# Performance work log

Measured on AMD Instinct MI355X. Metric: run time of the kernel, lower is better.

## Reference

```python
import jax, jax.numpy as jnp
import numpy as np

B, S, E, H, C = 2, 2048, 1024, 16, 16
SQ2 = np.float32(np.sqrt(2.0))


def setup_inputs() -> dict:
    key = jax.random.key(0)
    ks = jax.random.split(key, 32)
    sc = 0.02
    d = {"query": jax.random.normal(ks[0], (B, S, E), jnp.float32)}
    i = 1
    for dom in ("f", "w", "c"):
        d[f"Wp_{dom}"] = jax.random.normal(ks[i], (E, E), jnp.float32) * sc; i += 1
        d[f"bp_{dom}"] = jnp.zeros((E,), jnp.float32)
        d[f"Wc_{dom}"] = jax.random.normal(ks[i], (C, E, 3), jnp.float32) * sc; i += 1
        d[f"bc_{dom}"] = jnp.zeros((C,), jnp.float32)
        d["F" + dom] = jax.random.normal(ks[i], (C, E), jnp.float32); i += 1
    d["mha_iw"] = jax.random.normal(ks[i], (3 * E, E), jnp.float32) * sc; i += 1
    d["mha_ib"] = jnp.zeros((3 * E,), jnp.float32)
    d["mha_ow"] = jax.random.normal(ks[i], (E, E), jnp.float32) * sc; i += 1
    d["mha_ob"] = jnp.zeros((E,), jnp.float32)
    d["fus_W"] = jax.random.normal(ks[i], (E, 3 * E), jnp.float32) * sc; i += 1
    d["fus_b"] = jnp.zeros((E,), jnp.float32)
    return d


def _conv1d(x, W, b):
    # x: [B,S,E] real -> [B,S,C], conv over sequence, kernel 3, same padding
    y = jax.lax.conv_general_dilated(x.transpose(0, 2, 1), W, (1,), [(1, 1)],
                                     dimension_numbers=("NCH", "OIH", "NCH"))
    return (y + b[None, :, None]).transpose(0, 2, 1)


def _channels(x, Wc, bc, Fp):
    # spectral conv (real/imag separately if complex) + adaptive softmax filtering
    if jnp.iscomplexobj(x):
        ch = _conv1d(x.real, Wc, bc) + 1j * _conv1d(x.imag, Wc, bc)
    else:
        ch = _conv1d(x, Wc, bc)
    fw = jax.nn.softmax(Fp, axis=0)  # [C,E], softmax over channels
    return jnp.einsum("bsc,ce->bse", ch, fw.astype(ch.dtype))


def _spec_attn(q, k, v):
    scale = np.float32(1.0) / jnp.sqrt(jnp.asarray(q.shape[-1], jnp.float32))
    scores = jnp.einsum("bse,bte->bst", q, k) * scale
    if jnp.iscomplexobj(scores):
        w = jax.nn.softmax(scores.real, axis=-1)
        cw = (w * jnp.exp(1j * jnp.angle(scores))).astype(jnp.complex64)
        return jnp.einsum("bst,bte->bse", cw, v)
    return jnp.einsum("bst,bte->bse", jax.nn.softmax(scores, axis=-1), v)


def _haar(x):
    # simplified Haar wavelet transform; S is a power of 2 so no padding needed
    cur, coeffs = x, []
    while cur.shape[1] > 1:
        e, o = cur[:, 0::2, :], cur[:, 1::2, :]
        coeffs.append((e - o) / SQ2)
        cur = (e + o) / SQ2
    coeffs.append(cur)
    return jnp.concatenate(coeffs[::-1], axis=1)


def _dct_mats(L):
    n = jnp.arange(L, dtype=jnp.float32)
    k = n[:, None]
    D = jnp.cos(np.pi * k * (2.0 * n + 1.0) / (2.0 * L))
    D = D.at[0].multiply(np.float32(np.sqrt(1.0 / L)))
    D = D.at[1:].multiply(np.float32(np.sqrt(2.0 / L)))
    I = jnp.cos(np.pi * n * (2.0 * k + 1.0) / (2.0 * L))
    I = I.at[:, 0].multiply(np.float32(np.sqrt(1.0 / L)))
    I = I.at[:, 1:].multiply(np.float32(np.sqrt(2.0 / L)))
    return D, I


def _domain(x, Wp, bp, Wc, bc, Fp, domain):
    # key=value=query so q_domain == k_domain == v_domain
    xd = x @ Wp.T + bp
    if domain == "fourier":
        s = jnp.fft.fft(xd, axis=1)
        ch = _channels(s, Wc, bc, Fp)
        out = _spec_attn(ch, ch, ch)
        return jnp.fft.ifft(out, axis=1).real
    elif domain == "wavelet":
        s = _haar(xd)
        ch = _channels(s, Wc, bc, Fp)
        return _spec_attn(ch, ch, ch)  # inverse wavelet is identity in source
    else:  # cosine
        D, I = _dct_mats(xd.shape[1])
        s = jnp.einsum("st,bte->bse", D, xd)
        ch = _channels(s, Wc, bc, Fp)
        out = _spec_attn(ch, ch, ch)
        return jnp.einsum("st,bte->bse", I, out)


def _mha(x, iw, ib, ow, ob, nheads):
    # torch nn.MultiheadAttention (batch_first) self-attention
    Bx, L, Ex = x.shape
    hd = Ex // nheads
    qkv = x @ iw.T + ib
    q, k, v = jnp.split(qkv, 3, axis=-1)
    sh = lambda t: t.reshape(Bx, L, nheads, hd).transpose(0, 2, 1, 3)
    q, k, v = sh(q), sh(k), sh(v)
    a = jax.nn.softmax(jnp.einsum("bhld,bhmd->bhlm", q, k) / np.float32(np.sqrt(hd)), axis=-1)
    o = jnp.einsum("bhlm,bhmd->bhld", a, v).transpose(0, 2, 1, 3).reshape(Bx, L, Ex)
    return o @ ow.T + ob


def reference(query, Wp_f, bp_f, Wc_f, bc_f, Ff, Wp_w, bp_w, Wc_w, bc_w, Fw,
              Wp_c, bp_c, Wc_c, bc_c, Fc, mha_iw, mha_ib, mha_ow, mha_ob, fus_W, fus_b):
    outs = [
        _domain(query, Wp_f, bp_f, Wc_f, bc_f, Ff, "fourier"),
        _domain(query, Wp_w, bp_w, Wc_w, bc_w, Fw, "wavelet"),
        _domain(query, Wp_c, bp_c, Wc_c, bc_c, Fc, "cosine"),
    ]
    Bq, Sq, Eq = query.shape
    stacked = jnp.stack(outs, axis=2)                 # [B,S,3,E]
    corr = _mha(stacked.reshape(Bq * Sq, 3, Eq), mha_iw, mha_ib, mha_ow, mha_ob, H)
    fused = corr.reshape(Bq, Sq, 3 * Eq)              # concat of correlated domain outputs
    return fused @ fus_W.T + fus_b
```

## Files before the change

kernel.cpp:

```cpp
#include <hip/hip_runtime.h>
#include <cmath>

#define BB 2
#define SS_ 2048
#define EE 1024
#define CC 16

typedef __attribute__((ext_vector_type(8))) short short8v;
typedef __attribute__((ext_vector_type(4))) float floatx4;

__device__ __forceinline__ void split4(const float4 v, short4& h, short4& l)
{
    unsigned ux = __float_as_uint(v.x), uy = __float_as_uint(v.y);
    unsigned uz = __float_as_uint(v.z), uw = __float_as_uint(v.w);
    h.x = (short)(ux >> 16); h.y = (short)(uy >> 16);
    h.z = (short)(uz >> 16); h.w = (short)(uw >> 16);
    float lx = v.x - __uint_as_float(ux & 0xFFFF0000u);
    float ly = v.y - __uint_as_float(uy & 0xFFFF0000u);
    float lz = v.z - __uint_as_float(uz & 0xFFFF0000u);
    float lw = v.w - __uint_as_float(uw & 0xFFFF0000u);
    l.x = (short)(__float_as_uint(lx) >> 16);
    l.y = (short)(__float_as_uint(ly) >> 16);
    l.z = (short)(__float_as_uint(lz) >> 16);
    l.w = (short)(__float_as_uint(lw) >> 16);
}

#define BM 128
#define BN 128
#define BK 32
#define LDP 40

__launch_bounds__(256, 2)
__global__ void gemm_at(const float* __restrict__ A, const float* __restrict__ Bsrc,
                        float* __restrict__ C,
                        int K, int lda, int ldb, int ldc,
                        long sA, long sB, long sC, float alpha, int KS)
{
    __shared__ short sAh[BM * LDP], sAl[BM * LDP], sBh[BN * LDP], sBl[BN * LDP];
    const int z = blockIdx.z;
    const int bz = z / KS, ks = z % KS;
    const int klen = K / KS, kbase = ks * klen;
    A += (size_t)bz * sA; Bsrc += (size_t)bz * sB; C += (size_t)bz * sC;
    const int tid = threadIdx.x;
    const int m0 = blockIdx.y * BM, n0 = blockIdx.x * BN;

    const int lr0 = tid >> 3;
    const int kc0 = (tid & 7) * 4;
// ... 69 lines not shown
    }

    #pragma unroll
    for (int i = 0; i < 4; ++i) {
        const int mbase = m0 + wm * 64 + i * 16 + qd * 4;
        #pragma unroll
        for (int j = 0; j < 4; ++j) {
            const int n = n0 + wn * 64 + j * 16 + lr;
            #pragma unroll
            for (int r = 0; r < 4; ++r)
                atomicAdd(&C[(size_t)(mbase + r) * ldc + n], alpha * acc[i][j][r]);
        }
    }
}

template<int NT, int MODE>
__launch_bounds__(256, 4)
__global__ void skmfma(const float* __restrict__ A0, const float* __restrict__ A1,
                       const float* __restrict__ B0, const float* __restrict__ B1,
                       float* __restrict__ C0, float* __restrict__ C1,
                       int K, int lda, int ldb, int ldc,
                       long sA, long sB, long sC, float alpha, int KS)
{
    constexpr int NA = (MODE >= 1) ? 2 : 1;
    constexpr int NB = (MODE == 2) ? 2 : 1;
    constexpr int NACC = (MODE == 1) ? 2 : 1;
    constexpr int CT = NT / 16;
    __shared__ short sAh[NA][64 * 40], sAl[NA][64 * 40];
    __shared__ short sBh[NB][NT * 40], sBl[NB][NT * 40];
    const int z = blockIdx.z;
    const int zb = z / KS, ks = z % KS;
    const int klen = K / KS, kbase = ks * klen;
    const float* Ap[NA]; const float* Bp[NB]; float* Cp[NACC];
    Ap[0] = A0 + (size_t)zb * sA;
    if constexpr (NA == 2) Ap[1] = A1 + (size_t)zb * sA;
    Bp[0] = B0 + (size_t)zb * sB;
    if constexpr (NB == 2) Bp[1] = B1 + (size_t)zb * sB;
    Cp[0] = C0 + (size_t)zb * sC;
    if constexpr (NACC == 2) Cp[1] = C1 + (size_t)zb * sC;

    const int tid = threadIdx.x;
    const int m0 = blockIdx.x * 64;
    const int arow = tid >> 2, akc = (tid & 3) * 8;
    const int lane = tid & 63, w = tid >> 6;
    const int lr = lane & 15, qd = lane >> 4;

    floatx4 acc[NACC][CT];
    #pragma unroll
    for (int s = 0; s < NACC; ++s)
        #pragma unroll
        for (int j = 0; j < CT; ++j)
            acc[s][j] = (floatx4){0.f, 0.f, 0.f, 0.f};

    for (int kc = 0; kc < klen; kc += 32) {
        __syncthreads();
        #pragma unroll
        for (int s = 0; s < NA; ++s) {
            const float* pa = Ap[s] + (size_t)(m0 + arow) * lda + kbase + kc + akc;
            float4 v0 = *(const float4*)pa;
            float4 v1 = *(const float4*)(pa + 4);
            short4 h, l;
            split4(v0, h, l);
            *(short4*)&sAh[s][arow * 40 + akc] = h;
            *(short4*)&sAl[s][arow * 40 + akc] = l;
            split4(v1, h, l);
            *(short4*)&sAh[s][arow * 40 + akc + 4] = h;
            *(short4*)&sAl[s][arow * 40 + akc + 4] = l;
        }
        #pragma unroll
        for (int s = 0; s < NB; ++s) {
            for (int lin = tid; lin < 32 * (NT / 4); lin += 256) {
                int kk = lin / (NT / 4), n4 = (lin % (NT / 4)) * 4;
                float4 v = *(const float4*)(Bp[s] + (size_t)(kbase + kc + kk) * ldb + n4);
                short4 h, l; split4(v, h, l);
                sBh[s][(n4 + 0) * 40 + kk] = h.x; sBh[s][(n4 + 1) * 40 + kk] = h.y;
                sBh[s][(n4 + 2) * 40 + kk] = h.z; sBh[s][(n4 + 3) * 40 + kk] = h.w;
                sBl[s][(n4 + 0) * 40 + kk] = l.x; sBl[s][(n4 + 1) * 40 + kk] = l.y;
                sBl[s][(n4 + 2) * 40 + kk] = l.z; sBl[s][(n4 + 3) * 40 + kk] = l.w;
            }
        }
        __syncthreads();
        short8v ah[NA], alv[NA];
        #pragma unroll
        for (int s = 0; s < NA; ++s) {
            ah[s]  = *(const short8v*)&sAh[s][(w * 16 + lr) * 40 + qd * 8];
            alv[s] = *(const short8v*)&sAl[s][(w * 16 + lr) * 40 + qd * 8];
        }
        short8v bh[NB][CT], bl[NB][CT];
        #pragma unroll
        for (int s = 0; s < NB; ++s)
            #pragma unroll
            for (int j = 0; j < CT; ++j) {
                bh[s][j] = *(const short8v*)&sBh[s][(j * 16 + lr) * 40 + qd * 8];
                bl[s][j] = *(const short8v*)&sBl[s][(j * 16 + lr) * 40 + qd * 8];
            }
        if constexpr (MODE == 0) {
            #pragma unroll
            for (int j = 0; j < CT; ++j) {
                acc[0][j] = __builtin_amdgcn_mfma_f32_16x16x32_bf16(ah[0], bh[0][j], acc[0][j], 0, 0, 0);
                acc[0][j] = __builtin_amdgcn_mfma_f32_16x16x32_bf16(ah[0], bl[0][j], acc[0][j], 0, 0, 0);
                acc[0][j] = __builtin_amdgcn_mfma_f32_16x16x32_bf16(alv[0], bh[0][j], acc[0][j], 0, 0, 0);
            }
        } else if constexpr (MODE == 1) {
            #pragma unroll
            for (int j = 0; j < CT; ++j) {
                acc[0][j] = __builtin_amdgcn_mfma_f32_16x16x32_bf16(ah[0], bh[0][j], acc[0][j], 0, 0, 0);
                acc[0][j] = __builtin_amdgcn_mfma_f32_16x16x32_bf16(ah[0], bl[0][j], acc[0][j], 0, 0, 0);
                acc[0][j] = __builtin_amdgcn_mfma_f32_16x16x32_bf16(alv[0], bh[0][j], acc[0][j], 0, 0, 0);
                acc[1][j] = __builtin_amdgcn_mfma_f32_16x16x32_bf16(ah[1], bh[0][j], acc[1][j], 0, 0, 0);
                acc[1][j] = __builtin_amdgcn_mfma_f32_16x16x32_bf16(ah[1], bl[0][j], acc[1][j], 0, 0, 0);
                acc[1][j] = __builtin_amdgcn_mfma_f32_16x16x32_bf16(alv[1], bh[0][j], acc[1][j], 0, 0, 0);
            }
        } else {
            #pragma unroll
            for (int j = 0; j < CT; ++j) {
                acc[0][j] = __builtin_amdgcn_mfma_f32_16x16x32_bf16(ah[0], bh[0][j], acc[0][j], 0, 0, 0);
                acc[0][j] = __builtin_amdgcn_mfma_f32_16x16x32_bf16(ah[0], bl[0][j], acc[0][j], 0, 0, 0);
                acc[0][j] = __builtin_amdgcn_mfma_f32_16x16x32_bf16(alv[0], bh[0][j], acc[0][j], 0, 0, 0);
                acc[0][j] = __builtin_amdgcn_mfma_f32_16x16x32_bf16(ah[1], bh[1][j], acc[0][j], 0, 0, 0);
                acc[0][j] = __builtin_amdgcn_mfma_f32_16x16x32_bf16(ah[1], bl[1][j], acc[0][j], 0, 0, 0);
                acc[0][j] = __builtin_amdgcn_mfma_f32_16x16x32_bf16(alv[1], bh[1][j], acc[0][j], 0, 0, 0);
            }
        }
    }
    #pragma unroll
    for (int s = 0; s < NACC; ++s)
        #pragma unroll
        for (int j = 0; j < CT; ++j) {
            const int n = j * 16 + lr;
            const int mb = m0 + w * 16 + qd * 4;
            #pragma unroll
            for (int r = 0; r < 4; ++r)
                atomicAdd(&Cp[s][(size_t)(mb + r) * ldc + n], alpha * acc[s][j][r]);
        }
}

__global__ void gen_trig(float* __restrict__ Cc, float* __restrict__ Sn,
                         float* __restrict__ D, float* __restrict__ I)
{
    size_t idx = (size_t)blockIdx.x * 256 + threadIdx.x;
    if (idx < 4194304) {
        int k = (int)(idx >> 11);
        int n = (int)(idx & 2047);
        int m = (k * n) & 2047;
        float ang = (float)(6.283185307179586 * (double)m / 2048.0);
        Cc[idx] = cosf(ang);
        Sn[idx] = -sinf(ang);
    } else {
        idx -= 4194304;
        int i = (int)(idx >> 11);
        int j = (int)(idx & 2047);
        const float r1 = 0.022097086912079608f;
        const float r2 = 0.03125f;
        const float pif = 3.14159265358979323846f;
        float a  = (pif * (float)i) * (float)(2 * j + 1) / 4096.0f;
        D[idx] = cosf(a) * (i == 0 ? r1 : r2);
        float ai = (pif * (float)j) * (float)(2 * i + 1) / 4096.0f;
        I[idx] = cosf(ai) * (j == 0 ? r1 : r2);
    }
}
// ... 257 lines not shown
    #pragma unroll
    for (int c = 0; c < 16; ++c) {
        float cv = scr[row * 17 + c];
        float cvi = cplx ? sci[row * 17 + c] : 0.f;
        #pragma unroll
        for (int j = 0; j < 4; ++j) {
            float g = sG[c * 16 + ln * 4 + j];
            qp[j] = fmaf(cv, g, qp[j]);
            if (cplx) qpi[j] = fmaf(cvi, g, qpi[j]);
        }
    }
    *(float4*)(QR + ro) = *(float4*)&qp[0];
    if (cplx) *(float4*)(QI + ro) = *(float4*)&qpi[0];
}

__launch_bounds__(256)
__global__ void flash_all(const float* __restrict__ QpFr, const float* __restrict__ QpFi,
                          const float* __restrict__ chFr, const float* __restrict__ chFi,
                          float* __restrict__ OFr, float* __restrict__ OFi,
                          const float* __restrict__ QpW, const float* __restrict__ chW,
                          float* __restrict__ Ow_,
                          const float* __restrict__ QpC, const float* __restrict__ chC,
                          float* __restrict__ Oc_)
{
    const int dom = blockIdx.z;
    const int b = blockIdx.y;
    const int w = threadIdx.x >> 6, lane = threadIdx.x & 63;
    const int s = blockIdx.x * 4 + w;
    if (dom != 0) {
        const float* Qp = dom == 1 ? QpW : QpC;
        const float* ch = dom == 1 ? chW : chC;
        float* O = dom == 1 ? Ow_ : Oc_;
        const float* qrow = Qp + ((size_t)(b * 2048 + s)) * 16;
        float q[16];
        #pragma unroll
        for (int j = 0; j < 4; ++j) *(float4*)&q[j * 4] = *(const float4*)(qrow + j * 4);
        const float* chb = ch + (size_t)b * 2048 * 16;
        float m = -3.4e38f, l = 0.f;
        float acc[16] = {};
        for (int t = lane; t < 2048; t += 64) {
            const float* kp = chb + (size_t)t * 16;
            float kv[16];
            #pragma unroll
            for (int j = 0; j < 4; ++j) *(float4*)&kv[j * 4] = *(const float4*)(kp + j * 4);
            float sc = 0.f;
            #pragma unroll
            for (int e = 0; e < 16; ++e) sc = fmaf(q[e], kv[e], sc);
            float mn = fmaxf(m, sc);
            float al = __expf(m - mn), p = __expf(sc - mn);
            l = l * al + p;
            #pragma unroll
            for (int e = 0; e < 16; ++e) acc[e] = fmaf(acc[e], al, p * kv[e]);
            m = mn;
        }
        #pragma unroll
        for (int off = 1; off < 64; off <<= 1) {
            float m2 = __shfl_xor(m, off, 64);
            float l2 = __shfl_xor(l, off, 64);
            float mn = fmaxf(m, m2);
            float ra = __expf(m - mn), rb = __expf(m2 - mn);
            l = l * ra + l2 * rb;
            #pragma unroll
            for (int e = 0; e < 16; ++e) {
                float a2 = __shfl_xor(acc[e], off, 64);
                acc[e] = acc[e] * ra + a2 * rb;
            }
            m = mn;
        }
        if (lane < 4) {
            float inv = 1.f / l;
            float4 o4 = {acc[lane * 4] * inv, acc[lane * 4 + 1] * inv,
                         acc[lane * 4 + 2] * inv, acc[lane * 4 + 3] * inv};
            *(float4*)(O + ((size_t)(b * 2048 + s)) * 16 + lane * 4) = o4;
        }
        return;
    }
    float qr[16], qi[16];
    {
        const float* qrow = QpFr + ((size_t)(b * 2048 + s)) * 16;
        const float* qrowI = QpFi + ((size_t)(b * 2048 + s)) * 16;
        #pragma unroll
        for (int j = 0; j < 4; ++j) {
            *(float4*)&qr[j * 4] = *(const float4*)(qrow + j * 4);
            *(float4*)&qi[j * 4] = *(const float4*)(qrowI + j * 4);
        }
    }
    const float* cbR = chFr + (size_t)b * 2048 * 16;
    const float* cbI = chFi + (size_t)b * 2048 * 16;
    float m = -3.4e38f, l = 0.f;
    float aR[16] = {}, aI[16] = {};
    for (int t = lane; t < 2048; t += 64) {
        float kr[16], ki[16];
        #pragma unroll
        for (int j = 0; j < 4; ++j) {
            *(float4*)&kr[j * 4] = *(const float4*)(cbR + (size_t)t * 16 + j * 4);
            *(float4*)&ki[j * 4] = *(const float4*)(cbI + (size_t)t * 16 + j * 4);
        }
        float sre = 0.f, sim = 0.f;
        #pragma unroll
        for (int e = 0; e < 16; ++e) {
            sre = fmaf(qr[e], kr[e], sre); sre = fmaf(-qi[e], ki[e], sre);
            sim = fmaf(qr[e], ki[e], sim); sim = fmaf(qi[e], kr[e], sim);
        }
        float mn = fmaxf(m, sre);
        float al = __expf(m - mn), p = __expf(sre - mn);
        l = l * al + p;
        float rr = sqrtf(sre * sre + sim * sim);
        float iv = (rr > 0.f) ? (p / rr) : 0.f;
        float wr = (rr > 0.f) ? iv * sre : p;
        float wi = (rr > 0.f) ? iv * sim : 0.f;
        #pragma unroll
        for (int e = 0; e < 16; ++e) {
            aR[e] = fmaf(aR[e], al, wr * kr[e] - wi * ki[e]);
            aI[e] = fmaf(aI[e], al, wr * ki[e] + wi * kr[e]);
        }
        m = mn;
    }
    #pragma unroll
    for (int off = 1; off < 64; off <<= 1) {
        float m2 = __shfl_xor(m, off, 64);
        float l2 = __shfl_xor(l, off, 64);
        float mn = fmaxf(m, m2);
        float ra = __expf(m - mn), rb = __expf(m2 - mn);
        l = l * ra + l2 * rb;
        #pragma unroll
        for (int e = 0; e < 16; ++e) {
            float a2 = __shfl_xor(aR[e], off, 64);
            aR[e] = aR[e] * ra + a2 * rb;
            float b2 = __shfl_xor(aI[e], off, 64);
            aI[e] = aI[e] * ra + b2 * rb;
        }
        m = mn;
    }
    float inv = 1.f / l;
    size_t ro = ((size_t)(b * 2048 + s)) * 16;
    if (lane < 4) {
        float4 o4 = {aR[lane * 4] * inv, aR[lane * 4 + 1] * inv,
                     aR[lane * 4 + 2] * inv, aR[lane * 4 + 3] * inv};
        *(float4*)(OFr + ro + lane * 4) = o4;
    } else if (lane < 8) {
        int j = lane - 4;
        float4 o4 = {aI[j * 4] * inv, aI[j * 4 + 1] * inv,
                     aI[j * 4 + 2] * inv, aI[j * 4 + 3] * inv};
        *(float4*)(OFi + ro + j * 4) = o4;
    }
// ... 140 lines not shown
    float* Rf   = alloc(65536);
    float* Rc   = alloc(65536);
    float* Tw   = alloc(196608);
    float* chFr = alloc(65536); float* chFi = alloc(65536);
    float* QpFr = alloc(65536); float* QpFi = alloc(65536);
    float* chW  = alloc(65536); float* QpW  = alloc(65536);
    float* chC  = alloc(65536); float* QpC  = alloc(65536);
    float* OFr  = alloc(65536); float* OFi  = alloc(65536);
    float* Ow   = alloc(65536); float* Oc   = alloc(65536);
    float* Pt   = alloc(156672);
    float* Mten = alloc(41616);
    float* ybv  = alloc(1024);
    if (ws_size < off * sizeof(float)) return;

    float* Uf = Ucat, *Uw = Ucat + 196608, *Uc = Ucat + 2 * 196608;
    const long SE48 = 2048 * 48, SE16 = 2048 * 16;

    build_w2<<<dim3(576), dim3(256), 0, stream>>>(Wc[0], Wc[1], Wc[2], W2cat);
    prep_fw_G<<<dim3(3), dim3(256), 0, stream>>>(Fp[0], Fp[1], Fp[2], fwT, Gm);
    build_ub2<<<dim3(3), dim3(256), 0, stream>>>(bp[0], bp[1], bp[2], W2cat, ubv);
    build_yb2<<<dim3(256), dim3(256), 0, stream>>>(mha_ob, fus_W, fus_b, ybv);
    gen_trig<<<dim3(32768), dim3(256), 0, stream>>>(MAT0, MAT1, DCTD, DCTI);
    transpose_wp3<<<dim3(32, 32, 3), dim3(256), 0, stream>>>(Wp[0], Wp[1], Wp[2], WpT);
    init_all<<<dim3(34980), dim3(256), 0, stream>>>(W3cat, ubv, Pt, FTb, out, ybv);

    skmfma<48, 0><<<dim3(16, 1, 6), dim3(256), 0, stream>>>(
        WpT, nullptr, W2cat, nullptr, W3cat, nullptr,
        1024, 1024, 48, 48, 1048576, 49152, 49152, 1.f, 2);
    skmfma<48, 0><<<dim3(64, 1, 6), dim3(256), 0, stream>>>(
        query, nullptr, W3cat, nullptr, Ucat, nullptr,
        1024, 1024, 48, 48, 0, 49152, 196608, 1.f, 2);
    skmfma<48, 1><<<dim3(32, 1, 8), dim3(256), 0, stream>>>(
        MAT0, MAT1, Uf, nullptr, Tfr, Tfi,
        2048, 2048, 48, 48, 0, SE48, SE48, 1.f, 4);
    skmfma<48, 0><<<dim3(32, 1, 8), dim3(256), 0, stream>>>(
        DCTD, nullptr, Uc, nullptr, Tc, nullptr,
        2048, 2048, 48, 48, 0, SE48, SE48, 1.f, 4);

    haar_all<<<dim3(12, 2), dim3(256), 0, stream>>>(Uw, Tw);

    conv_all<<<dim3(32, 2, 3), dim3(256), 0, stream>>>(
        Tfr, Tfi, Tw, Tc, Gm, bc[0], bc[1], bc[2],
        chFr, chFi, chW, chC, QpFr, QpFi, QpW, QpC);

    flash_all<<<dim3(512, 2, 3), dim3(256), 0, stream>>>(
        QpFr, QpFi, chFr, chFi, OFr, OFi, QpW, chW, Ow, QpC, chC, Oc);

    skmfma<16, 2><<<dim3(32, 1, 8), dim3(256), 0, stream>>>(
        MAT0, MAT1, OFr, OFi, Rf, nullptr,
        2048, 2048, 16, 16, 0, SE16, SE16, 1.f / 2048.f, 4);
    skmfma<16, 0><<<dim3(32, 1, 8), dim3(256), 0, stream>>>(
        DCTI, nullptr, Oc, nullptr, Rc, nullptr,
        2048, 2048, 16, 16, 0, SE16, SE16, 1.f, 4);
    skmfma<16, 0><<<dim3(48, 1, 6), dim3(256), 0, stream>>>(
        mha_iw, nullptr, fwT, nullptr, Pt, nullptr,
        1024, 1024, 16, 17, 0, 16384, 52224, 1.f, 2);

    ib_append<<<dim3(36), dim3(256), 0, stream>>>(mha_ib, Pt);
    build_M<<<dim3(144), dim3(256), 0, stream>>>(Pt, Mten);

    mha_o<<<dim3(16, 16), dim3(256), 0, stream>>>(Rf, Ow, Rc, Pt, Mten, MO);

    transpose_k<<<dim3(32, 32), dim3(256), 0, stream>>>(mha_ow, OWT, 1024, 1024);
    gemm_at<<<dim3(8, 8, 6), dim3(256), 0, stream>>>(
        fus_W, OWT, FTb, 1024, 3072, 1024, 3072, 1024, 0, 1024, 1.f, 2);

    gemm_at<<<dim3(8, 32, 2), dim3(256), 0, stream>>>(
        MO, FTb, out, 3072, 3072, 3072, 1024, 0, 0, 0, 1.f, 2);
}
```

Before: 765.7 us.

## Merge skinny GEMM launches, restructure flash attention, raise split-K and occupancy

Replaces the templated skinny MFMA kernel with specialized kernels that merge the forward Fourier and DCT transforms, and the inverse transforms plus the MHA projection, into single launches. This cuts launch count and lets the groups run concurrently. The flash attention kernels are rewritten to handle two query rows per wave and to process keys in blocks of 256 with one max rescale per block instead of one per key. The large GEMMs double their split-K factor and raise launch bounds to 4 blocks per SM, which adds atomic traffic and register pressure.

New measurement: 979.3 us. +27.9%, slower.

```diff
diff --git a/kernel.cpp b/kernel.cpp
--- a/kernel.cpp
+++ b/kernel.cpp
@@ -30,7 +30,7 @@
 #define BK 32
 #define LDP 40
 
-__launch_bounds__(256, 2)
+__launch_bounds__(256, 4)
 __global__ void gemm_at(const float* __restrict__ A, const float* __restrict__ Bsrc,
                         float* __restrict__ C,
                         int K, int lda, int ldb, int ldc,
@@ -130,125 +130,281 @@
     }
 }
 
-template<int NT, int MODE>
 __launch_bounds__(256, 4)
-__global__ void skmfma(const float* __restrict__ A0, const float* __restrict__ A1,
-                       const float* __restrict__ B0, const float* __restrict__ B1,
-                       float* __restrict__ C0, float* __restrict__ C1,
-                       int K, int lda, int ldb, int ldc,
-                       long sA, long sB, long sC, float alpha, int KS)
-{
-    constexpr int NA = (MODE >= 1) ? 2 : 1;
-    constexpr int NB = (MODE == 2) ? 2 : 1;
-    constexpr int NACC = (MODE == 1) ? 2 : 1;
-    constexpr int CT = NT / 16;
-    __shared__ short sAh[NA][64 * 40], sAl[NA][64 * 40];
-    __shared__ short sBh[NB][NT * 40], sBl[NB][NT * 40];
+__global__ void sk48(const float* __restrict__ A, const float* __restrict__ B,
+                     float* __restrict__ C, int lda,
+                     long sA, long sB, long sC, int KS)
+{
+    __shared__ short sAh[64 * 40], sAl[64 * 40];
+    __shared__ short sBh[48 * 40], sBl[48 * 40];
     const int z = blockIdx.z;
     const int zb = z / KS, ks = z % KS;
-    const int klen = K / KS, kbase = ks * klen;
-    const float* Ap[NA]; const float* Bp[NB]; float* Cp[NACC];
-    Ap[0] = A0 + (size_t)zb * sA;
-    if constexpr (NA == 2) Ap[1] = A1 + (size_t)zb * sA;
-    Bp[0] = B0 + (size_t)zb * sB;
-    if constexpr (NB == 2) Bp[1] = B1 + (size_t)zb * sB;
-    Cp[0] = C0 + (size_t)zb * sC;
-    if constexpr (NACC == 2) Cp[1] = C1 + (size_t)zb * sC;
-
+    const int kbase = ks * 512;
+    A += (size_t)zb * sA; B += (size_t)zb * sB; C += (size_t)zb * sC;
     const int tid = threadIdx.x;
     const int m0 = blockIdx.x * 64;
     const int arow = tid >> 2, akc = (tid & 3) * 8;
     const int lane = tid & 63, w = tid >> 6;
     const int lr = lane & 15, qd = lane >> 4;
 
-    floatx4 acc[NACC][CT];
-    #pragma unroll
-    for (int s = 0; s < NACC; ++s)
-        #pragma unroll
-        for (int j = 0; j < CT; ++j)
-            acc[s][j] = (floatx4){0.f, 0.f, 0.f, 0.f};
-
-    for (int kc = 0; kc < klen; kc += 32) {
+    floatx4 acc[3];
+    #pragma unroll
+    for (int j = 0; j < 3; ++j) acc[j] = (floatx4){0.f, 0.f, 0.f, 0.f};
+
+    for (int kc = 0; kc < 512; kc += 32) {
         __syncthreads();
-        #pragma unroll
-        for (int s = 0; s < NA; ++s) {
-            const float* pa = Ap[s] + (size_t)(m0 + arow) * lda + kbase + kc + akc;
-            float4 v0 = *(const float4*)pa;
-            float4 v1 = *(const float4*)(pa + 4);
+        {
+            const float* pa = A + (size_t)(m0 + arow) * lda + kbase + kc + akc;
+            float4 v0 = *(const float4*)pa, v1 = *(const float4*)(pa + 4);
             short4 h, l;
             split4(v0, h, l);
-            *(short4*)&sAh[s][arow * 40 + akc] = h;
-            *(short4*)&sAl[s][arow * 40 + akc] = l;
+            *(short4*)&sAh[arow * 40 + akc] = h;
+            *(short4*)&sAl[arow * 40 + akc] = l;
             split4(v1, h, l);
-            *(short4*)&sAh[s][arow * 40 + akc + 4] = h;
-            *(short4*)&sAl[s][arow * 40 + akc + 4] = l;
-        }
-        #pragma unroll
-        for (int s = 0; s < NB; ++s) {
-            for (int lin = tid; lin < 32 * (NT / 4); lin += 256) {
-                int kk = lin / (NT / 4), n4 = (lin % (NT / 4)) * 4;
-                float4 v = *(const float4*)(Bp[s] + (size_t)(kbase + kc + kk) * ldb + n4);
-                short4 h, l; split4(v, h, l);
-                sBh[s][(n4 + 0) * 40 + kk] = h.x; sBh[s][(n4 + 1) * 40 + kk] = h.y;
-                sBh[s][(n4 + 2) * 40 + kk] = h.z; sBh[s][(n4 + 3) * 40 + kk] = h.w;
-                sBl[s][(n4 + 0) * 40 + kk] = l.x; sBl[s][(n4 + 1) * 40 + kk] = l.y;
-                sBl[s][(n4 + 2) * 40 + kk] = l.z; sBl[s][(n4 + 3) * 40 + kk] = l.w;
+            *(short4*)&sAh[arow * 40 + akc + 4] = h;
+            *(short4*)&sAl[arow * 40 + akc + 4] = l;
+        }
+        for (int lin = tid; lin < 384; lin += 256) {
+            int kk = lin / 12, n4 = (lin % 12) * 4;
+            float4 v = *(const float4*)(B + (size_t)(kbase + kc + kk) * 48 + n4);
+            short4 h, l; split4(v, h, l);
+            sBh[(n4 + 0) * 40 + kk] = h.x; sBh[(n4 + 1) * 40 + kk] = h.y;
+            sBh[(n4 + 2) * 40 + kk] = h.z; sBh[(n4 + 3) * 40 + kk] = h.w;
+            sBl[(n4 + 0) * 40 + kk] = l.x; sBl[(n4 + 1) * 40 + kk] = l.y;
+            sBl[(n4 + 2) * 40 + kk] = l.z; sBl[(n4 + 3) * 40 + kk] = l.w;
+        }
+        __syncthreads();
+        short8v ah = *(const short8v*)&sAh[(w * 16 + lr) * 40 + qd * 8];
+        short8v al = *(const short8v*)&sAl[(w * 16 + lr) * 40 + qd * 8];
+        #pragma unroll
+        for (int j = 0; j < 3; ++j) {
+            short8v bh = *(const short8v*)&sBh[(j * 16 + lr) * 40 + qd * 8];
+            short8v bl = *(const short8v*)&sBl[(j * 16 + lr) * 40 + qd * 8];
+            acc[j] = __builtin_amdgcn_mfma_f32_16x16x32_bf16(ah, bh, acc[j], 0, 0, 0);
+            acc[j] = __builtin_amdgcn_mfma_f32_16x16x32_bf16(ah, bl, acc[j], 0, 0, 0);
+            acc[j] = __builtin_amdgcn_mfma_f32_16x16x32_bf16(al, bh, acc[j], 0, 0, 0);
+        }
+    }
+    #pragma unroll
+    for (int j = 0; j < 3; ++j) {
+        const int n = j * 16 + lr;
+        const int mb = m0 + w * 16 + qd * 4;
+        #pragma unroll
+        for (int r = 0; r < 4; ++r)
+            atomicAdd(&C[(size_t)(mb + r) * 48 + n], acc[j][r]);
+    }
+}
+
+__launch_bounds__(256, 4)
+__global__ void skinny_fwd(const float* __restrict__ MAT0, const float* __restrict__ MAT1,
+                           const float* __restrict__ DCTD,
+                           const float* __restrict__ Uf, const float* __restrict__ Uc,
+                           float* __restrict__ Tfr, float* __restrict__ Tfi,
+                           float* __restrict__ Tc)
+{
+    __shared__ short sAh[2][64 * 40], sAl[2][64 * 40];
+    __shared__ short sBh[48 * 40], sBl[48 * 40];
+    const int z = blockIdx.z;
+    const bool dual = (z < 8);
+    const int zz = dual ? z : z - 8;
+    const int zb = zz >> 2, ks = zz & 3;
+    const int kbase = ks * 512;
+    const float* A0 = dual ? MAT0 : DCTD;
+    const float* Bp = (dual ? Uf : Uc) + (size_t)zb * 98304;
+    float* C0 = (dual ? Tfr : Tc) + (size_t)zb * 98304;
+    float* C1 = Tfi + (size_t)zb * 98304;
+
+    const int tid = threadIdx.x;
+    const int m0 = blockIdx.x * 64;
+    const int arow = tid >> 2, akc = (tid & 3) * 8;
+    const int lane = tid & 63, w = tid >> 6;
+    const int lr = lane & 15, qd = lane >> 4;
+
+    floatx4 acc0[3], acc1[3];
+    #pragma unroll
+    for (int j = 0; j < 3; ++j) {
+        acc0[j] = (floatx4){0.f, 0.f, 0.f, 0.f};
+        acc1[j] = (floatx4){0.f, 0.f, 0.f, 0.f};
+    }
+
+    for (int kc = 0; kc < 512; kc += 32) {
+        __syncthreads();
+        {
+            const float* pa = A0 + (size_t)(m0 + arow) * 2048 + kbase + kc + akc;
+            float4 v0 = *(const float4*)pa, v1 = *(const float4*)(pa + 4);
+            short4 h, l;
+            split4(v0, h, l);
+            *(short4*)&sAh[0][arow * 40 + akc] = h;
+            *(short4*)&sAl[0][arow * 40 + akc] = l;
+            split4(v1, h, l);
+            *(short4*)&sAh[0][arow * 40 + akc + 4] = h;
+            *(short4*)&sAl[0][arow * 40 + akc + 4] = l;
+        }
+        if (dual) {
+            const float* pa = MAT1 + (size_t)(m0 + arow) * 2048 + kbase + kc + akc;
+            float4 v0 = *(const float4*)pa, v1 = *(const float4*)(pa + 4);
+            short4 h, l;
+            split4(v0, h, l);
+            *(short4*)&sAh[1][arow * 40 + akc] = h;
+            *(short4*)&sAl[1][arow * 40 + akc] = l;
+            split4(v1, h, l);
+            *(short4*)&sAh[1][arow * 40 + akc + 4] = h;
+            *(short4*)&sAl[1][arow * 40 + akc + 4] = l;
+        }
+        for (int lin = tid; lin < 384; lin += 256) {
+            int kk = lin / 12, n4 = (lin % 12) * 4;
+            float4 v = *(const float4*)(Bp + (size_t)(kbase + kc + kk) * 48 + n4);
+            short4 h, l; split4(v, h, l);
+            sBh[(n4 + 0) * 40 + kk] = h.x; sBh[(n4 + 1) * 40 + kk] = h.y;
+            sBh[(n4 + 2) * 40 + kk] = h.z; sBh[(n4 + 3) * 40 + kk] = h.w;
+            sBl[(n4 + 0) * 40 + kk] = l.x; sBl[(n4 + 1) * 40 + kk] = l.y;
+            sBl[(n4 + 2) * 40 + kk] = l.z; sBl[(n4 + 3) * 40 + kk] = l.w;
+        }
+        __syncthreads();
+        short8v ah0 = *(const short8v*)&sAh[0][(w * 16 + lr) * 40 + qd * 8];
+        short8v al0 = *(const short8v*)&sAl[0][(w * 16 + lr) * 40 + qd * 8];
+        short8v bh[3], bl[3];
+        #pragma unroll
+        for (int j = 0; j < 3; ++j) {
+            bh[j] = *(const short8v*)&sBh[(j * 16 + lr) * 40 + qd * 8];
+            bl[j] = *(const short8v*)&sBl[(j * 16 + lr) * 40 + qd * 8];
+        }
+        #pragma unroll
+        for (int j = 0; j < 3; ++j) {
+            acc0[j] = __builtin_amdgcn_mfma_f32_16x16x32_bf16(ah0, bh[j], acc0[j], 0, 0, 0);
+            acc0[j] = __builtin_amdgcn_mfma_f32_16x16x32_bf16(ah0, bl[j], acc0[j], 0, 0, 0);
+            acc0[j] = __builtin_amdgcn_mfma_f32_16x16x32_bf16(al0, bh[j], acc0[j], 0, 0, 0);
+        }
+        if (dual) {
+            short8v ah1 = *(const short8v*)&sAh[1][(w * 16 + lr) * 40 + qd * 8];
+            short8v al1 = *(const short8v*)&sAl[1][(w * 16 + lr) * 40 + qd * 8];
+            #pragma unroll
+            for (int j = 0; j < 3; ++j) {
+                acc1[j] = __builtin_amdgcn_mfma_f32_16x16x32_bf16(ah1, bh[j], acc1[j], 0, 0, 0);
+                acc1[j] = __builtin_amdgcn_mfma_f32_16x16x32_bf16(ah1, bl[j], acc1[j], 0, 0, 0);
+                acc1[j] = __builtin_amdgcn_mfma_f32_16x16x32_bf16(al1, bh[j], acc1[j], 0, 0, 0);
             }
         }
+    }
+    #pragma unroll
+    for (int j = 0; j < 3; ++j) {
+        const int n = j * 16 + lr;
+        const int mb = m0 + w * 16 + qd * 4;
+        #pragma unroll
+        for (int r = 0; r < 4; ++r) {
+            atomicAdd(&C0[(size_t)(mb + r) * 48 + n], acc0[j][r]);
+            if (dual) atomicAdd(&C1[(size_t)(mb + r) * 48 + n], acc1[j][r]);
+        }
+    }
+}
+
+__launch_bounds__(256, 4)
+__global__ void skinny_inv(const float* __restrict__ MAT0, const float* __restrict__ MAT1,
+                           const float* __restrict__ DCTI,
+                           const float* __restrict__ OFr, const float* __restrict__ OFi,
+                           const float* __restrict__ Oc,
+                           const float* __restrict__ iw, const float* __restrict__ fwT,
+                           float* __restrict__ Rf, float* __restrict__ Rc,
+                           float* __restrict__ Pt)
+{
+    __shared__ short sAh[2][64 * 40], sAl[2][64 * 40];
+    __shared__ short sBh[2][16 * 40], sBl[2][16 * 40];
+    const int z = blockIdx.z;
+    const int mode = (z < 8) ? 0 : ((z < 16) ? 1 : 2);
+    if (mode < 2 && blockIdx.x >= 32) return;
+    const float *A0, *A1 = nullptr, *B0, *B1 = nullptr;
+    float* C; float alpha; int lda, ldc, kbase;
+    if (mode == 0) {
+        int zb = z >> 2, ks = z & 3;
+        kbase = ks * 512; lda = 2048;
+        A0 = MAT0; A1 = MAT1;
+        B0 = OFr + (size_t)zb * 32768; B1 = OFi + (size_t)zb * 32768;
+        C = Rf + (size_t)zb * 32768; ldc = 16; alpha = 1.f / 2048.f;
+    } else if (mode == 1) {
+        int zz = z - 8; int zb = zz >> 2, ks = zz & 3;
+        kbase = ks * 512; lda = 2048;
+        A0 = DCTI; B0 = Oc + (size_t)zb * 32768;
+        C = Rc + (size_t)zb * 32768; ldc = 16; alpha = 1.f;
+    } else {
+        int zz = z - 16; int l = zz >> 1, ks = zz & 1;
+        kbase = ks * 512; lda = 1024;
+        A0 = iw; B0 = fwT + (size_t)l * 16384;
+        C = Pt + (size_t)l * 52224; ldc = 17; alpha = 1.f;
+    }
+    const bool dual = (mode == 0);
+
+    const int tid = threadIdx.x;
+    const int m0 = blockIdx.x * 64;
+    const int arow = tid >> 2, akc = (tid & 3) * 8;
+    const int lane = tid & 63, w = tid >> 6;
+    const int lr = lane & 15, qd = lane >> 4;
+
+    floatx4 acc = (floatx4){0.f, 0.f, 0.f, 0.f};
+
+    for (int kc = 0; kc < 512; kc += 32) {
         __syncthreads();
-        short8v ah[NA], alv[NA];
-        #pragma unroll
-        for (int s = 0; s < NA; ++s) {
-            ah[s]  = *(const short8v*)&sAh[s][(w * 16 + lr) * 40 + qd * 8];
-            alv[s] = *(const short8v*)&sAl[s][(w * 16 + lr) * 40 + qd * 8];
-        }
-        short8v bh[NB][CT], bl[NB][CT];
-        #pragma unroll
-        for (int s = 0; s < NB; ++s)
-            #pragma unroll
-            for (int j = 0; j < CT; ++j) {
-                bh[s][j] = *(const short8v*)&sBh[s][(j * 16 + lr) * 40 + qd * 8];
-                bl[s][j] = *(const short8v*)&sBl[s][(j * 16 + lr) * 40 + qd * 8];
-            }
-        if constexpr (MODE == 0) {
-            #pragma unroll
-            for (int j = 0; j < CT; ++j) {
-                acc[0][j] = __builtin_amdgcn_mfma_f32_16x16x32_bf16(ah[0], bh[0][j], acc[0][j], 0, 0, 0);
-                acc[0][j] = __builtin_amdgcn_mfma_f32_16x16x32_bf16(ah[0], bl[0][j], acc[0][j], 0, 0, 0);
-                acc[0][j] = __builtin_amdgcn_mfma_f32_16x16x32_bf16(alv[0], bh[0][j], acc[0][j], 0, 0, 0);
-            }
-        } else if constexpr (MODE == 1) {
-            #pragma unroll
-            for (int j = 0; j < CT; ++j) {
-                acc[0][j] = __builtin_amdgcn_mfma_f32_16x16x32_bf16(ah[0], bh[0][j], acc[0][j], 0, 0, 0);
-                acc[0][j] = __builtin_amdgcn_mfma_f32_16x16x32_bf16(ah[0], bl[0][j], acc[0][j], 0, 0, 0);
-                acc[0][j] = __builtin_amdgcn_mfma_f32_16x16x32_bf16(alv[0], bh[0][j], acc[0][j], 0, 0, 0);
-                acc[1][j] = __builtin_amdgcn_mfma_f32_16x16x32_bf16(ah[1], bh[0][j], acc[1][j], 0, 0, 0);
-                acc[1][j] = __builtin_amdgcn_mfma_f32_16x16x32_bf16(ah[1], bl[0][j], acc[1][j], 0, 0, 0);
-                acc[1][j] = __builtin_amdgcn_mfma_f32_16x16x32_bf16(alv[1], bh[0][j], acc[1][j], 0, 0, 0);
-            }
-        } else {
-            #pragma unroll
-            for (int j = 0; j < CT; ++j) {
-                acc[0][j] = __builtin_amdgcn_mfma_f32_16x16x32_bf16(ah[0], bh[0][j], acc[0][j], 0, 0, 0);
-                acc[0][j] = __builtin_amdgcn_mfma_f32_16x16x32_bf16(ah[0], bl[0][j], acc[0][j], 0, 0, 0);
-                acc[0][j] = __builtin_amdgcn_mfma_f32_16x16x32_bf16(alv[0], bh[0][j], acc[0][j], 0, 0, 0);
-                acc[0][j] = __builtin_amdgcn_mfma_f32_16x16x32_bf16(ah[1], bh[1][j], acc[0][j], 0, 0, 0);
-                acc[0][j] = __builtin_amdgcn_mfma_f32_16x16x32_bf16(ah[1], bl[1][j], acc[0][j], 0, 0, 0);
-                acc[0][j] = __builtin_amdgcn_mfma_f32_16x16x32_bf16(alv[1], bh[1][j], acc[0][j], 0, 0, 0);
-            }
-        }
-    }
-    #pragma unroll
-    for (int s = 0; s < NACC; ++s)
-        #pragma unroll
-        for (int j = 0; j < CT; ++j) {
-            const int n = j * 16 + lr;
-            const int mb = m0 + w * 16 + qd * 4;
-            #pragma unroll
-            for (int r = 0; r < 4; ++r)
-                atomicAdd(&Cp[s][(size_t)(mb + r) * ldc + n], alpha * acc[s][j][r]);
-        }
+        {
+            const float* pa = A0 + (size_t)(m0 + arow) * lda + kbase + kc + akc;
+            float4 v0 = *(const float4*)pa, v1 = *(const float4*)(pa + 4);
+            short4 h, l;
+            split4(v0, h, l);
+            *(short4*)&sAh[0][arow * 40 + akc] = h;
+            *(short4*)&sAl[0][arow * 40 + akc] = l;
+            split4(v1, h, l);
+            *(short4*)&sAh[0][arow * 40 + akc + 4] = h;
+            *(short4*)&sAl[0][arow * 40 + akc + 4] = l;
+        }
+        if (dual) {
+            const float* pa = A1 + (size_t)(m0 + arow) * lda + kbase + kc + akc;
+            float4 v0 = *(const float4*)pa, v1 = *(const float4*)(pa + 4);
+            short4 h, l;
+            split4(v0, h, l);
+            *(short4*)&sAh[1][arow * 40 + akc] = h;
+            *(short4*)&sAl[1][arow * 40 + akc] = l;
+            split4(v1, h, l);
+            *(short4*)&sAh[1][arow * 40 + akc + 4] = h;
+            *(short4*)&sAl[1][arow * 40 + akc + 4] = l;
+        }
+        if (tid < 128) {
+            int kk = tid >> 2, n4 = (tid & 3) * 4;
+            float4 v = *(const float4*)(B0 + (size_t)(kbase + kc + kk) * 16 + n4);
+            short4 h, l; split4(v, h, l);
+            sBh[0][(n4 + 0) * 40 + kk] = h.x; sBh[0][(n4 + 1) * 40 + kk] = h.y;
+            sBh[0][(n4 + 2) * 40 + kk] = h.z; sBh[0][(n4 + 3) * 40 + kk] = h.w;
+            sBl[0][(n4 + 0) * 40 + kk] = l.x; sBl[0][(n4 + 1) * 40 + kk] = l.y;
+            sBl[0][(n4 + 2) * 40 + kk] = l.z; sBl[0][(n4 + 3) * 40 + kk] = l.w;
+        } else if (dual) {
+            int t2 = tid - 128;
+            int kk = t2 >> 2, n4 = (t2 & 3) * 4;
+            float4 v = *(const float4*)(B1 + (size_t)(kbase + kc + kk) * 16 + n4);
+            short4 h, l; split4(v, h, l);
+            sBh[1][(n4 + 0) * 40 + kk] = h.x; sBh[1][(n4 + 1) * 40 + kk] = h.y;
+            sBh[1][(n4 + 2) * 40 + kk] = h.z; sBh[1][(n4 + 3) * 40 + kk] = h.w;
+            sBl[1][(n4 + 0) * 40 + kk] = l.x; sBl[1][(n4 + 1) * 40 + kk] = l.y;
+            sBl[1][(n4 + 2) * 40 + kk] = l.z; sBl[1][(n4 + 3) * 40 + kk] = l.w;
+        }
+        __syncthreads();
+        short8v ah0 = *(const short8v*)&sAh[0][(w * 16 + lr) * 40 + qd * 8];
+        short8v al0 = *(const short8v*)&sAl[0][(w * 16 + lr) * 40 + qd * 8];
+        short8v bh0 = *(const short8v*)&sBh[0][lr * 40 + qd * 8];
+        short8v bl0 = *(const short8v*)&sBl[0][lr * 40 + qd * 8];
+        acc = __builtin_amdgcn_mfma_f32_16x16x32_bf16(ah0, bh0, acc, 0, 0, 0);
+        acc = __builtin_amdgcn_mfma_f32_16x16x32_bf16(ah0, bl0, acc, 0, 0, 0);
+        acc = __builtin_amdgcn_mfma_f32_16x16x32_bf16(al0, bh0, acc, 0, 0, 0);
+        if (dual) {
+            short8v ah1 = *(const short8v*)&sAh[1][(w * 16 + lr) * 40 + qd * 8];
+            short8v al1 = *(const short8v*)&sAl[1][(w * 16 + lr) * 40 + qd * 8];
+            short8v bh1 = *(const short8v*)&sBh[1][lr * 40 + qd * 8];
+            short8v bl1 = *(const short8v*)&sBl[1][lr * 40 + qd * 8];
+            acc = __builtin_amdgcn_mfma_f32_16x16x32_bf16(ah1, bh1, acc, 0, 0, 0);
+            acc = __builtin_amdgcn_mfma_f32_16x16x32_bf16(ah1, bl1, acc, 0, 0, 0);
+            acc = __builtin_amdgcn_mfma_f32_16x16x32_bf16(al1, bh1, acc, 0, 0, 0);
+        }
+    }
+    const int mb = m0 + w * 16 + qd * 4;
+    #pragma unroll
+    for (int r = 0; r < 4; ++r)
+        atomicAdd(&C[(size_t)(mb + r) * ldc + lr], alpha * acc[r]);
 }
 
 __global__ void gen_trig(float* __restrict__ Cc, float* __restrict__ Sn,
@@ -259,7 +415,7 @@
         int k = (int)(idx >> 11);
         int n = (int)(idx & 2047);
         int m = (k * n) & 2047;
-        float ang = (float)(6.283185307179586 * (double)m / 2048.0);
+        float ang = (float)((double)m * 0.0030679615757712823);
         Cc[idx] = cosf(ang);
         Sn[idx] = -sinf(ang);
     } else {
@@ -547,67 +703,143 @@
     if (cplx) *(float4*)(QI + ro) = *(float4*)&qpi[0];
 }
 
+__device__ __forceinline__ float dot16(const float q[16], const float k[16])
+{
+    float a = q[0] * k[0], b = q[1] * k[1], c = q[2] * k[2], d = q[3] * k[3];
+    a = fmaf(q[4], k[4], a);  b = fmaf(q[5], k[5], b);
+    c = fmaf(q[6], k[6], c);  d = fmaf(q[7], k[7], d);
+    a = fmaf(q[8], k[8], a);  b = fmaf(q[9], k[9], b);
+    c = fmaf(q[10], k[10], c); d = fmaf(q[11], k[11], d);
+    a = fmaf(q[12], k[12], a); b = fmaf(q[13], k[13], b);
+    c = fmaf(q[14], k[14], c); d = fmaf(q[15], k[15], d);
+    return (a + b) + (c + d);
+}
+
+__device__ __forceinline__ void cdot16(const float qr[16], const float qi[16],
+                                       const float kr[16], const float ki[16],
+                                       float& sre, float& sim)
+{
+    float a = 0.f, b = 0.f, c = 0.f, d = 0.f;
+    float e2 = 0.f, f = 0.f, g = 0.f, h = 0.f;
+    #pragma unroll
+    for (int e = 0; e < 8; ++e) {
+        a = fmaf(qr[e], kr[e], a);
+        b = fmaf(qr[e + 8], kr[e + 8], b);
+        c = fmaf(qi[e], ki[e], c);
+        d = fmaf(qi[e + 8], ki[e + 8], d);
+        e2 = fmaf(qr[e], ki[e], e2);
+        f = fmaf(qr[e + 8], ki[e + 8], f);
+        g = fmaf(qi[e], kr[e], g);
+        h = fmaf(qi[e + 8], kr[e + 8], h);
+    }
+    sre = (a + b) - (c + d);
+    sim = (e2 + f) + (g + h);
+}
+
 __launch_bounds__(256)
-__global__ void flash_all(const float* __restrict__ QpFr, const float* __restrict__ QpFi,
-                          const float* __restrict__ chFr, const float* __restrict__ chFi,
-                          float* __restrict__ OFr, float* __restrict__ OFi,
-                          const float* __restrict__ QpW, const float* __restrict__ chW,
-                          float* __restrict__ Ow_,
-                          const float* __restrict__ QpC, const float* __restrict__ chC,
-                          float* __restrict__ Oc_)
-{
-    const int dom = blockIdx.z;
-    const int b = blockIdx.y;
+__global__ void flash_v4(const float* __restrict__ QpFr, const float* __restrict__ QpFi,
+                         const float* __restrict__ chFr, const float* __restrict__ chFi,
+                         float* __restrict__ OFr, float* __restrict__ OFi,
+                         const float* __restrict__ QpW, const float* __restrict__ chW,
+                         float* __restrict__ Ow_,
+                         const float* __restrict__ QpC, const float* __restrict__ chC,
+                         float* __restrict__ Oc_)
+{
+    const int dom = blockIdx.z, b = blockIdx.y;
     const int w = threadIdx.x >> 6, lane = threadIdx.x & 63;
-    const int s = blockIdx.x * 4 + w;
     if (dom != 0) {
+        if (blockIdx.x >= 256) return;
         const float* Qp = dom == 1 ? QpW : QpC;
         const float* ch = dom == 1 ? chW : chC;
         float* O = dom == 1 ? Ow_ : Oc_;
-        const float* qrow = Qp + ((size_t)(b * 2048 + s)) * 16;
-        float q[16];
-        #pragma unroll
-        for (int j = 0; j < 4; ++j) *(float4*)&q[j * 4] = *(const float4*)(qrow + j * 4);
+        const int s0 = blockIdx.x * 8 + w * 2;
+        float q0[16], q1[16];
+        {
+            const float* qr0 = Qp + ((size_t)(b * 2048 + s0)) * 16;
+            #pragma unroll
+            for (int j = 0; j < 4; ++j) {
+                *(float4*)&q0[j * 4] = *(const float4*)(qr0 + j * 4);
+                *(float4*)&q1[j * 4] = *(const float4*)(qr0 + 16 + j * 4);
+            }
+        }
         const float* chb = ch + (size_t)b * 2048 * 16;
-        float m = -3.4e38f, l = 0.f;
-        float acc[16] = {};
-        for (int t = lane; t < 2048; t += 64) {
-            const float* kp = chb + (size_t)t * 16;
-            float kv[16];
-            #pragma unroll
-            for (int j = 0; j < 4; ++j) *(float4*)&kv[j * 4] = *(const float4*)(kp + j * 4);
-            float sc = 0.f;
-            #pragma unroll
-            for (int e = 0; e < 16; ++e) sc = fmaf(q[e], kv[e], sc);
-            float mn = fmaxf(m, sc);
-            float al = __expf(m - mn), p = __expf(sc - mn);
-            l = l * al + p;
-            #pragma unroll
-            for (int e = 0; e < 16; ++e) acc[e] = fmaf(acc[e], al, p * kv[e]);
-            m = mn;
+        float m0 = -3.4e38f, m1 = -3.4e38f, l0 = 0.f, l1 = 0.f;
+        float a0[16] = {}, a1[16] = {};
+        for (int t0 = 0; t0 < 2048; t0 += 512) {
+            float sv0[8], sv1[8];
+            #pragma unroll
+            for (int j = 0; j < 8; ++j) {
+                const float* kp = chb + (size_t)(t0 + j * 64 + lane) * 16;
+                float kv[16];
+                #pragma unroll
+                for (int i = 0; i < 4; ++i) *(float4*)&kv[i * 4] = *(const float4*)(kp + i * 4);
+                sv0[j] = dot16(q0, kv);
+                sv1[j] = dot16(q1, kv);
+            }
+            float tm0 = fmaxf(fmaxf(fmaxf(sv0[0], sv0[1]), fmaxf(sv0[2], sv0[3])),
+                              fmaxf(fmaxf(sv0[4], sv0[5]), fmaxf(sv0[6], sv0[7])));
+            float tm1 = fmaxf(fmaxf(fmaxf(sv1[0], sv1[1]), fmaxf(sv1[2], sv1[3])),
+                              fmaxf(fmaxf(sv1[4], sv1[5]), fmaxf(sv1[6], sv1[7])));
+            float nm0 = fmaxf(m0, tm0), nm1 = fmaxf(m1, tm1);
+            float al0 = __expf(m0 - nm0), al1 = __expf(m1 - nm1);
+            l0 *= al0; l1 *= al1;
+            #pragma unroll
+            for (int e = 0; e < 16; ++e) { a0[e] *= al0; a1[e] *= al1; }
+            m0 = nm0; m1 = nm1;
+            #pragma unroll
+            for (int j = 0; j < 8; ++j) {
+                const float* kp = chb + (size_t)(t0 + j * 64 + lane) * 16;
+                float kv[16];
+                #pragma unroll
+                for (int i = 0; i < 4; ++i) *(float4*)&kv[i * 4] = *(const float4*)(kp + i * 4);
+                float p0 = __expf(sv0[j] - m0);
+                float p1 = __expf(sv1[j] - m1);
+                l0 += p0; l1 += p1;
+                #pragma unroll
+                for (int e = 0; e < 16; ++e) {
+                    a0[e] = fmaf(p0, kv[e], a0[e]);
+                    a1[e] = fmaf(p1, kv[e], a1[e]);
+                }
+            }
         }
         #pragma unroll
         for (int off = 1; off < 64; off <<= 1) {
-            float m2 = __shfl_xor(m, off, 64);
-            float l2 = __shfl_xor(l, off, 64);
-            float mn = fmaxf(m, m2);
-            float ra = __expf(m - mn), rb = __expf(m2 - mn);
-            l = l * ra + l2 * rb;
+            float mm = __shfl_xor(m0, off, 64), ll = __shfl_xor(l0, off, 64);
+            float mn = fmaxf(m0, mm);
+            float ra = __expf(m0 - mn), rb = __expf(mm - mn);
+            l0 = l0 * ra + ll * rb;
             #pragma unroll
             for (int e = 0; e < 16; ++e) {
-                float a2 = __shfl_xor(acc[e], off, 64);
-                acc[e] = acc[e] * ra + a2 * rb;
+                float x = __shfl_xor(a0[e], off, 64);
+                a0[e] = a0[e] * ra + x * rb;
             }
-            m = mn;
+            m0 = mn;
+            mm = __shfl_xor(m1, off, 64); ll = __shfl_xor(l1, off, 64);
+            mn = fmaxf(m1, mm);
+            ra = __expf(m1 - mn); rb = __expf(mm - mn);
+            l1 = l1 * ra + ll * rb;
+            #pragma unroll
+            for (int e = 0; e < 16; ++e) {
+                float x = __shfl_xor(a1[e], off, 64);
+                a1[e] = a1[e] * ra + x * rb;
+            }
+            m1 = mn;
         }
         if (lane < 4) {
-            float inv = 1.f / l;
-            float4 o4 = {acc[lane * 4] * inv, acc[lane * 4 + 1] * inv,
-                         acc[lane * 4 + 2] * inv, acc[lane * 4 + 3] * inv};
-            *(float4*)(O + ((size_t)(b * 2048 + s)) * 16 + lane * 4) = o4;
+            float inv = 1.f / l0;
+            float4 o4 = {a0[lane * 4] * inv, a0[lane * 4 + 1] * inv,
+                         a0[lane * 4 + 2] * inv, a0[lane * 4 + 3] * inv};
+            *(float4*)(O + ((size_t)(b * 2048 + s0)) * 16 + lane * 4) = o4;
+        } else if (lane < 8) {
+            int j = lane - 4;
+            float inv = 1.f / l1;
+            float4 o4 = {a1[j * 4] * inv, a1[j * 4 + 1] * inv,
+                         a1[j * 4 + 2] * inv, a1[j * 4 + 3] * inv};
+            *(float4*)(O + ((size_t)(b * 2048 + s0 + 1)) * 16 + j * 4) = o4;
         }
         return;
     }
+    const int s = blockIdx.x * 4 + w;
     float qr[16], qi[16];
     {
         const float* qrow = QpFr + ((size_t)(b * 2048 + s)) * 16;
@@ -622,32 +854,49 @@
     const float* cbI = chFi + (size_t)b * 2048 * 16;
     float m = -3.4e38f, l = 0.f;
     float aR[16] = {}, aI[16] = {};
-    for (int t = lane; t < 2048; t += 64) {
-        float kr[16], ki[16];
+    for (int t0 = 0; t0 < 2048; t0 += 256) {
+        float svr[4], svi[4];
         #pragma unroll
         for (int j = 0; j < 4; ++j) {
-            *(float4*)&kr[j * 4] = *(const float4*)(cbR + (size_t)t * 16 + j * 4);
-            *(float4*)&ki[j * 4] = *(const float4*)(cbI + (size_t)t * 16 + j * 4);
-        }
-        float sre = 0.f, sim = 0.f;
-        #pragma unroll
-        for (int e = 0; e < 16; ++e) {
-            sre = fmaf(qr[e], kr[e], sre); sre = fmaf(-qi[e], ki[e], sre);
-            sim = fmaf(qr[e], ki[e], sim); sim = fmaf(qi[e], kr[e], sim);
-        }
-        float mn = fmaxf(m, sre);
-        float al = __expf(m - mn), p = __expf(sre - mn);
-        l = l * al + p;
-        float rr = sqrtf(sre * sre + sim * sim);
-        float iv = (rr > 0.f) ? (p / rr) : 0.f;
-        float wr = (rr > 0.f) ? iv * sre : p;
-        float wi = (rr > 0.f) ? iv * sim : 0.f;
-        #pragma unroll
-        for (int e = 0; e < 16; ++e) {
-            aR[e] = fmaf(aR[e], al, wr * kr[e] - wi * ki[e]);
-            aI[e] = fmaf(aI[e], al, wr * ki[e] + wi * kr[e]);
-        }
-        m = mn;
+            const size_t ko = (size_t)(t0 + j * 64 + lane) * 16;
+            float kr[16], ki[16];
+            #pragma unroll
+            for (int i = 0; i < 4; ++i) {
+                *(float4*)&kr[i * 4] = *(const float4*)(cbR + ko + i * 4);
+                *(float4*)&ki[i * 4] = *(const float4*)(cbI + ko + i * 4);
+            }
+            cdot16(qr, qi, kr, ki, svr[j], svi[j]);
+        }
+        float tm = fmaxf(fmaxf(svr[0], svr[1]), fmaxf(svr[2], svr[3]));
+        float nm = fmaxf(m, tm);
+        float al = __expf(m - nm);
+        l *= al;
+        #pragma unroll
+        for (int e = 0; e < 16; ++e) { aR[e] *= al; aI[e] *= al; }
+        m = nm;
+        #pragma unroll
+        for (int j = 0; j < 4; ++j) {
+            const size_t ko = (size_t)(t0 + j * 64 + lane) * 16;
+            float kr[16], ki[16];
+            #pragma unroll
+            for (int i = 0; i < 4; ++i) {
+                *(float4*)&kr[i * 4] = *(const float4*)(cbR + ko + i * 4);
+                *(float4*)&ki[i * 4] = *(const float4*)(cbI + ko + i * 4);
+            }
+            float p = __expf(svr[j] - m);
+            l += p;
+            float rr = sqrtf(svr[j] * svr[j] + svi[j] * svi[j]);
+            float iv = (rr > 0.f) ? (p / rr) : 0.f;
+            float wr = (rr > 0.f) ? iv * svr[j] : p;
+            float wi = (rr > 0.f) ? iv * svi[j] : 0.f;
+            #pragma unroll
+            for (int e = 0; e < 16; ++e) {
+                aR[e] = fmaf(wr, kr[e], aR[e]);
+                aR[e] = fmaf(-wi, ki[e], aR[e]);
+                aI[e] = fmaf(wr, ki[e], aI[e]);
+                aI[e] = fmaf(wi, kr[e], aI[e]);
+            }
+        }
     }
     #pragma unroll
     for (int off = 1; off < 64; off <<= 1) {
@@ -658,10 +907,10 @@
         l = l * ra + l2 * rb;
         #pragma unroll
         for (int e = 0; e < 16; ++e) {
-            float a2 = __shfl_xor(aR[e], off, 64);
-            aR[e] = aR[e] * ra + a2 * rb;
-            float b2 = __shfl_xor(aI[e], off, 64);
-            aI[e] = aI[e] * ra + b2 * rb;
+            float x = __shfl_xor(aR[e], off, 64);
+            aR[e] = aR[e] * ra + x * rb;
+            float y = __shfl_xor(aI[e], off, 64);
+            aI[e] = aI[e] * ra + y * rb;
         }
         m = mn;
     }
@@ -832,7 +1081,6 @@
     if (ws_size < off * sizeof(float)) return;
 
     float* Uf = Ucat, *Uw = Ucat + 196608, *Uc = Ucat + 2 * 196608;
-    const long SE48 = 2048 * 48, SE16 = 2048 * 16;
 
     build_w2<<<dim3(576), dim3(256), 0, stream>>>(Wc[0], Wc[1], Wc[2], W2cat);
     prep_fw_G<<<dim3(3), dim3(256), 0, stream>>>(Fp[0], Fp[1], Fp[2], fwT, Gm);
@@ -842,18 +1090,13 @@
     transpose_wp3<<<dim3(32, 32, 3), dim3(256), 0, stream>>>(Wp[0], Wp[1], Wp[2], WpT);
     init_all<<<dim3(34980), dim3(256), 0, stream>>>(W3cat, ubv, Pt, FTb, out, ybv);
 
-    skmfma<48, 0><<<dim3(16, 1, 6), dim3(256), 0, stream>>>(
-        WpT, nullptr, W2cat, nullptr, W3cat, nullptr,
-        1024, 1024, 48, 48, 1048576, 49152, 49152, 1.f, 2);
-    skmfma<48, 0><<<dim3(64, 1, 6), dim3(256), 0, stream>>>(
-        query, nullptr, W3cat, nullptr, Ucat, nullptr,
-        1024, 1024, 48, 48, 0, 49152, 196608, 1.f, 2);
-    skmfma<48, 1><<<dim3(32, 1, 8), dim3(256), 0, stream>>>(
-        MAT0, MAT1, Uf, nullptr, Tfr, Tfi,
-        2048, 2048, 48, 48, 0, SE48, SE48, 1.f, 4);
-    skmfma<48, 0><<<dim3(32, 1, 8), dim3(256), 0, stream>>>(
-        DCTD, nullptr, Uc, nullptr, Tc, nullptr,
-        2048, 2048, 48, 48, 0, SE48, SE48, 1.f, 4);
+    sk48<<<dim3(16, 1, 6), dim3(256), 0, stream>>>(
+        WpT, W2cat, W3cat, 1024, 1048576, 49152, 49152, 2);
+    sk48<<<dim3(64, 1, 6), dim3(256), 0, stream>>>(
+        query, W3cat, Ucat, 1024, 0, 49152, 196608, 2);
+
+    skinny_fwd<<<dim3(32, 1, 16), dim3(256), 0, stream>>>(
+        MAT0, MAT1, DCTD, Uf, Uc, Tfr, Tfi, Tc);
 
     haar_all<<<dim3(12, 2), dim3(256), 0, stream>>>(Uw, Tw);
 
@@ -861,18 +1104,11 @@
         Tfr, Tfi, Tw, Tc, Gm, bc[0], bc[1], bc[2],
         chFr, chFi, chW, chC, QpFr, QpFi, QpW, QpC);
 
-    flash_all<<<dim3(512, 2, 3), dim3(256), 0, stream>>>(
+    flash_v4<<<dim3(512, 2, 3), dim3(256), 0, stream>>>(
         QpFr, QpFi, chFr, chFi, OFr, OFi, QpW, chW, Ow, QpC, chC, Oc);
 
-    skmfma<16, 2><<<dim3(32, 1, 8), dim3(256), 0, stream>>>(
-        MAT0, MAT1, OFr, OFi, Rf, nullptr,
-        2048, 2048, 16, 16, 0, SE16, SE16, 1.f / 2048.f, 4);
-    skmfma<16, 0><<<dim3(32, 1, 8), dim3(256), 0, stream>>>(
-        DCTI, nullptr, Oc, nullptr, Rc, nullptr,
-        2048, 2048, 16, 16, 0, SE16, SE16, 1.f, 4);
-    skmfma<16, 0><<<dim3(48, 1, 6), dim3(256), 0, stream>>>(
-        mha_iw, nullptr, fwT, nullptr, Pt, nullptr,
-        1024, 1024, 16, 17, 0, 16384, 52224, 1.f, 2);
+    skinny_inv<<<dim3(48, 1, 22), dim3(256), 0, stream>>>(
+        MAT0, MAT1, DCTI, OFr, OFi, Oc, mha_iw, fwT, Rf, Rc, Pt);
 
     ib_append<<<dim3(36), dim3(256), 0, stream>>>(mha_ib, Pt);
     build_M<<<dim3(144), dim3(256), 0, stream>>>(Pt, Mten);
@@ -880,9 +1116,9 @@
     mha_o<<<dim3(16, 16), dim3(256), 0, stream>>>(Rf, Ow, Rc, Pt, Mten, MO);
 
     transpose_k<<<dim3(32, 32), dim3(256), 0, stream>>>(mha_ow, OWT, 1024, 1024);
-    gemm_at<<<dim3(8, 8, 6), dim3(256), 0, stream>>>(
-        fus_W, OWT, FTb, 1024, 3072, 1024, 3072, 1024, 0, 1024, 1.f, 2);
-
-    gemm_at<<<dim3(8, 32, 2), dim3(256), 0, stream>>>(
-        MO, FTb, out, 3072, 3072, 3072, 1024, 0, 0, 0, 1.f, 2);
-}
+    gemm_at<<<dim3(8, 8, 12), dim3(256), 0, stream>>>(
+        fus_W, OWT, FTb, 1024, 3072, 1024, 3072, 1024, 0, 1024, 1.f, 4);
+
+    gemm_at<<<dim3(8, 32, 4), dim3(256), 0, stream>>>(
+        MO, FTb, out, 3072, 3072, 3072, 1024, 0, 0, 0, 1.f, 4);
+}
```
